# Kernel optimization log

Hardware: AMD Instinct MI355X
Metric: run time of the kernel (lower is better)

Reference implementation:

```python
import jax, jax.numpy as jnp
import numpy as np

C_IN = 128      # pair channel
C_HID = 32      # per-head hidden dim
H = 4           # heads
INF = 1e9
LN_EPS = 1e-5


def setup_inputs() -> dict:
    key = jax.random.key(0)
    ks = jax.random.split(key, 8)
    B, N = 1, 256
    s = 0.02
    return {
        "x": jax.random.normal(ks[0], (B, N, N, C_IN), dtype=jnp.float32),
        "mask": jnp.ones((B, N, N), dtype=jnp.float32),
        "ln_w": jnp.ones((C_IN,), dtype=jnp.float32),
        "ln_b": jnp.zeros((C_IN,), dtype=jnp.float32),
        "w_b": jax.random.normal(ks[1], (H, C_IN), dtype=jnp.float32) * s,      # triangle-bias linear (no bias)
        "w_q": jax.random.normal(ks[2], (H * C_HID, C_IN), dtype=jnp.float32) * s,
        "w_k": jax.random.normal(ks[3], (H * C_HID, C_IN), dtype=jnp.float32) * s,
        "w_v": jax.random.normal(ks[4], (H * C_HID, C_IN), dtype=jnp.float32) * s,
        "w_g": jax.random.normal(ks[5], (H * C_HID, C_IN), dtype=jnp.float32) * s,
        "b_g": jnp.ones((H * C_HID,), dtype=jnp.float32),
        "w_o": jax.random.normal(ks[6], (C_IN, H * C_HID), dtype=jnp.float32) * s,
        "b_o": jnp.zeros((C_IN,), dtype=jnp.float32),
    }


def reference(x, mask, ln_w, ln_b, w_b, w_q, w_k, w_v, w_g, b_g, w_o, b_o):
    # starting=True -> no transpose
    # LayerNorm over channel dim
    mu = jnp.mean(x, axis=-1, keepdims=True)
    var = jnp.var(x, axis=-1, keepdims=True)
    xn = (x - mu) * jax.lax.rsqrt(var + LN_EPS) * ln_w + ln_b            # [B,I,J,C]

    # mask bias: [B, I, 1, 1, J]
    mask_bias = (INF * (mask - 1.0))[..., :, None, None, :]

    # triangle bias: linear -> [B,I,J,H] -> permute -> [B,H,I,J] -> [B,1,H,I,J]
    tri_bias = jnp.einsum("bijc,hc->bhij", xn, w_b)[:, None]

    # QKV projections, per-head: weights reshaped to [H, D, C]
    Wq = w_q.reshape(H, C_HID, C_IN)
    Wk = w_k.reshape(H, C_HID, C_IN)
    Wv = w_v.reshape(H, C_HID, C_IN)
    scale = 1.0 / np.sqrt(C_HID)
    q = jnp.einsum("bijc,hdc->bihjd", xn, Wq) * scale                    # [B,I,H,J,D]
    k = jnp.einsum("bijc,hdc->bihjd", xn, Wk)
    v = jnp.einsum("bijc,hdc->bihjd", xn, Wv)

    # attention over the J (column) axis of each row i
    a = jnp.einsum("bihqd,bihkd->bihqk", q, k) + mask_bias + tri_bias    # [B,I,H,J,J]
    a = jax.nn.softmax(a, axis=-1)
    o = jnp.einsum("bihqk,bihkd->biqhd", a, v)                           # [B,I,J,H,D]

    # sigmoid gating
    g = jax.nn.sigmoid(jnp.einsum("bijc,ec->bije", xn, w_g) + b_g)       # [B,I,J,H*D]
    o = o.reshape(*o.shape[:-2], H * C_HID) * g

    # output projection
    return jnp.einsum("bije,ce->bijc", o, w_o) + b_o                     # [B,I,J,C_in]
```

## Files before the change

kernel.cpp:

```cpp
#include <hip/hip_runtime.h>

#define N 256
#define C 128
#define H 4
#define D 32
#define NP (N*N)
#define LN_EPS 1e-5f
#define LOG2E 1.4426950408889634f

using f32x4 = __attribute__((ext_vector_type(4))) float;
using bf8   = __attribute__((ext_vector_type(8))) short;
using u16x4 = __attribute__((ext_vector_type(4))) unsigned short;

__device__ __forceinline__ float bf2f(ushort u) {
    union { uint u; float f; } v; v.u = ((uint)u) << 16; return v.f;
}
__device__ __forceinline__ ushort f2bf(float f) {
    union { float f; uint u; } v; v.f = f;
    uint u = v.u;
    u += 0x7fffu + ((u >> 16) & 1u);
    return (ushort)(u >> 16);
}
__device__ __forceinline__ ushort f2bf_trunc(float f) {
    union { float f; uint u; } v; v.f = f;
    return (ushort)(v.u >> 16);
}

__global__ __launch_bounds__(256) void prep_weights(
    const float* __restrict__ wq, const float* __restrict__ wk,
    const float* __restrict__ wv, const float* __restrict__ wg,
    const float* __restrict__ wb, const float* __restrict__ wo,
    ushort* __restrict__ Wcat, ushort* __restrict__ WbPad, ushort* __restrict__ Wo)
{
    int t = blockIdx.x * 256 + threadIdx.x;
    const float scale = 0.17677669529663689f * LOG2E;
    float v;
    if (t < 16384)       v = wq[t] * scale;
    else if (t < 32768)  v = wk[t - 16384];
    else if (t < 49152)  v = wv[t - 32768];
    else                 v = wg[t - 49152];
    Wcat[t] = f2bf(v);
    if (t < 16384) Wo[t] = f2bf(wo[t]);
    if (t < 2048)  WbPad[t] = (t < 512) ? f2bf(wb[t]) : (ushort)0;
}

__global__ __launch_bounds__(512, 4) void ln_proj(
    const float* __restrict__ x, const float* __restrict__ lnw,
    const float* __restrict__ lnb, const ushort* __restrict__ Wcat,
    const ushort* __restrict__ WbPad, const float* __restrict__ bg,
    ushort* __restrict__ qb, ushort* __restrict__ kb,
    ushort* __restrict__ vbT, ushort* __restrict__ gate,
    ushort* __restrict__ tri_p)
{
    __shared__ ushort At[128 * 128];
    __shared__ ushort Bt[128 * 128];
    int mt = blockIdx.x;
    int t  = threadIdx.x;
    int wave = t >> 6, lane = t & 63;
    int lane32 = lane & 31, rsel = lane >> 5;

    {
        const float4 w4 = ((const float4*)lnw)[lane32];
        const float4 b4 = ((const float4*)lnb)[lane32];
        const float* xb = x + (size_t)mt * 128 * C;
        #pragma unroll
        for (int pp = 0; pp < 8; pp++) {
            int r = pp * 16 + wave * 2 + rsel;
            float4 xv = ((const float4*)(xb + r * C))[lane32];
            float s  = xv.x + xv.y + xv.z + xv.w;
            float ss = xv.x*xv.x + xv.y*xv.y + xv.z*xv.z + xv.w*xv.w;
            #pragma unroll
            for (int m = 1; m < 32; m <<= 1) {
                s  += __shfl_xor(s, m, 64);
                ss += __shfl_xor(ss, m, 64);
            }
            float mean = s * (1.f / 128.f);
            float var  = ss * (1.f / 128.f) - mean * mean;
            float rstd = rsqrtf(var + LN_EPS);
            u16x4 o;
            o[0] = f2bf((xv.x - mean) * rstd * w4.x + b4.x);
            o[1] = f2bf((xv.y - mean) * rstd * w4.y + b4.y);
            o[2] = f2bf((xv.z - mean) * rstd * w4.z + b4.z);
            o[3] = f2bf((xv.w - mean) * rstd * w4.w + b4.w);
            int c8 = lane32 >> 1;
            int chunk = r * 16 + (c8 ^ (r & 7));
            *(u16x4*)&At[chunk * 8 + (lane32 & 1) * 4] = o;
        }
    }
    __syncthreads();

    int lrow = lane & 15, quad = lane >> 4;
    int wr = wave >> 1, wc = wave & 1;

    bf8 afr[4][2];
    #pragma unroll
    for (int ks = 0; ks < 4; ks++) {
        int c8 = ks * 4 + quad;
        #pragma unroll
        for (int mi = 0; mi < 2; mi++) {
            int row = wr * 32 + mi * 16 + lrow;
            afr[ks][mi] = *(const bf8*)&At[(row * 16 + (c8 ^ (row & 7))) * 8];
        }
    }

    {
        f32x4 at0 = (f32x4){0.f,0.f,0.f,0.f}, at1 = (f32x4){0.f,0.f,0.f,0.f};
        #pragma unroll
        for (int ks = 0; ks < 4; ks++) {
            int c8 = ks * 4 + quad;
            bf8 bt = *(const bf8*)(WbPad + lrow * C + c8 * 8);
            at0 = __builtin_amdgcn_mfma_f32_16x16x32_bf16(afr[ks][0], bt, at0, 0, 0, 0);
            at1 = __builtin_amdgcn_mfma_f32_16x16x32_bf16(afr[ks][1], bt, at1, 0, 0, 0);
        }
        if (wc == 0 && lrow < 4) {
            int q = mt >> 1;
            int qc = q >> 4, quadq = (q >> 2) & 3, rr = q & 3;
            #pragma unroll
            for (int mi = 0; mi < 2; mi++) {
                #pragma unroll
                for (int r = 0; r < 4; r++) {
                    int k = (mt & 1) * 128 + wr * 32 + mi * 16 + quad * 4 + r;
                    int n = k >> 4, lk = k & 15;
                    int lanet = quadq * 16 + lk;
                    int v = n * 4 + rr, j = v >> 3, m2 = v & 7;
                    float val = (mi == 0) ? at0[r] : at1[r];
                    tri_p[lrow * 65536 + ((qc * 8 + j) * 64 + lanet) * 8 + m2] =
                        f2bf(val * LOG2E);
                }
            }
        }
    }

    uint4 breg[4];
    {
        const uint4* Bg = (const uint4*)Wcat;
        #pragma unroll
        for (int ii = 0; ii < 4; ii++) breg[ii] = Bg[t + ii * 512];
    }

    #pragma unroll 1
    for (int nt = 0; nt < 4; nt++) {
        __syncthreads();
        #pragma unroll
        for (int ii = 0; ii < 4; ii++) {
            int idx = t + ii * 512;
            int row = idx >> 4, c8 = idx & 15;
            ((uint4*)Bt)[row * 16 + (c8 ^ (row & 7))] = breg[ii];
        }
        __syncthreads();
        if (nt < 3) {
            const uint4* Bg = (const uint4*)(Wcat + (size_t)(nt + 1) * 128 * C);
            #pragma unroll
            for (int ii = 0; ii < 4; ii++) breg[ii] = Bg[t + ii * 512];
        }

        f32x4 acc[2][4];
        #pragma unroll
        for (int mi = 0; mi < 2; mi++)
            #pragma unroll
            for (int ni = 0; ni < 4; ni++) acc[mi][ni] = (f32x4){0.f, 0.f, 0.f, 0.f};

        #pragma unroll
        for (int ks = 0; ks < 4; ks++) {
            int c8 = ks * 4 + quad;
            bf8 b[4];
            #pragma unroll
            for (int ni = 0; ni < 4; ni++) {
                int row = wc * 64 + ni * 16 + lrow;
                b[ni] = *(const bf8*)&Bt[(row * 16 + (c8 ^ (row & 7))) * 8];
            }
            #pragma unroll
            for (int mi = 0; mi < 2; mi++)
                #pragma unroll
                for (int ni = 0; ni < 4; ni++)
                    acc[mi][ni] = __builtin_amdgcn_mfma_f32_16x16x32_bf16(afr[ks][mi], b[ni], acc[mi][ni], 0, 0, 0);
        }

        if (nt == 2) {
            __syncthreads();
            #pragma unroll
            for (int mi = 0; mi < 2; mi++) {
                #pragma unroll
                for (int ni = 0; ni < 4; ni++) {
                    int col = wc * 64 + ni * 16 + lrow;
                    #pragma unroll
                    for (int r = 0; r < 4; r++) {
                        int keyl = wr * 32 + mi * 16 + quad * 4 + r;
                        Bt[col * 128 + (keyl ^ (lrow << 3))] = f2bf(acc[mi][ni][r]);
                    }
                }
            }
            __syncthreads();
            int i_row = mt >> 1;
            #pragma unroll
            for (int itr = 0; itr < 4; itr++) {
                int oidx = itr * 512 + t;
                int col = oidx >> 4, kc = oidx & 15;
                bf8 val = *(const bf8*)&Bt[col * 128 + ((kc * 8) ^ ((col & 15) << 3))];
                *(bf8*)&vbT[(size_t)(i_row * 128 + col) * N + (mt & 1) * 128 + kc * 8] = val;
            }
        } else {
            ushort* dst = (nt == 0) ? qb : (nt == 1) ? kb : gate;
            bool gated = (nt == 3);
            #pragma unroll
            for (int mi = 0; mi < 2; mi++) {
                #pragma unroll
                for (int ni = 0; ni < 4; ni++) {
                    int col = wc * 64 + ni * 16 + lrow;
                    #pragma unroll
                    for (int r = 0; r < 4; r++) {
                        int row = mt * 128 + wr * 32 + mi * 16 + quad * 4 + r;
                        float vv = acc[mi][ni][r];
                        if (gated) vv = 1.f / (1.f + __expf(-(vv + bg[col])));
                        dst[(size_t)row * C + col] = f2bf(vv);
                    }
                }
            }
        }
    }
}

__global__ __launch_bounds__(512, 4) void attn_kernel(
    const ushort* __restrict__ qb, const ushort* __restrict__ kb,
    const ushort* __restrict__ vbT, const ushort* __restrict__ tri_p,
    const float* __restrict__ mask, ushort* __restrict__ ob)
{
    __shared__ ushort Kf[8192];
    __shared__ ushort Vf[8192];
    __shared__ ushort Pf[8][2048];

    int i  = blockIdx.x;
    int h  = blockIdx.y;
    int t  = threadIdx.x;
    int wave = t >> 6, lane = t & 63;
    int lrow = lane & 15, quad = lane >> 4;

    {
        const ushort* kt = kb + (size_t)(i * N) * C + h * D;
        #pragma unroll
        for (int it = 0; it < 2; it++) {
            int idx = it * 512 + t;
            int key = idx >> 2, d0 = (idx & 3) * 8;
            bf8 kv = *(const bf8*)(kt + (size_t)key * C + d0);
            int c = (idx >> 6) * 64 + (idx & 3) * 16 + ((idx >> 2) & 15);
            *(bf8*)&Kf[c * 8] = kv;
        }
    }
    {
        const ushort* vt = vbT + (size_t)((i * H + h) * D) * N;
        #pragma unroll
        for (int it = 0; it < 2; it++) {
            int idx = it * 512 + t;
            bf8 vv = *(const bf8*)(vt + idx * 8);
            int c = (idx >> 9) * 512 + ((idx >> 2) & 7) * 64 + (idx & 3) * 16 + ((idx >> 5) & 15);
            c ^= (c >> 6) & 7;
            *(bf8*)&Vf[c * 8] = vv;
        }
    }
    float mb[16];
    #pragma unroll
    for (int n = 0; n < 16; n++)
        mb[n] = (1e9f * LOG2E) * (mask[i * N + n * 16 + lrow] - 1.0f);
    __syncthreads();

    ushort* Pw = &Pf[wave][0];
    const ushort* trih = tri_p + (size_t)h * 65536;
    int pq = quad * 32 + (lrow & 7);
    int l3 = (lrow >> 3) & 1;

    #pragma unroll 1
    for (int cc = 0; cc < 2; cc++) {
        int qc = wave * 2 + cc;
        bf8 aq = *(const bf8*)(qb + (size_t)(i * N + qc * 16 + lrow) * C + h * D + quad * 8);
        float sum[4] = {0.f, 0.f, 0.f, 0.f};
        f32x4 o[2];
        o[0] = (f32x4){0.f, 0.f, 0.f, 0.f};
        o[1] = (f32x4){0.f, 0.f, 0.f, 0.f};

        #pragma unroll
        for (int half = 0; half < 2; half++) {
            f32x4 s8[8];
            #pragma unroll
            for (int n8 = 0; n8 < 8; n8++) {
                bf8 kf = *(const bf8*)&Kf[((half * 8 + n8) * 64 + lane) * 8];
                s8[n8] = __builtin_amdgcn_mfma_f32_16x16x32_bf16(
                    aq, kf, (f32x4){0.f, 0.f, 0.f, 0.f}, 0, 0, 0);
            }
            const ushort* tp = trih + ((size_t)(qc * 8 + half * 4) * 64 + lane) * 8;
            bf8 tf[4];
            #pragma unroll
            for (int jj = 0; jj < 4; jj++)
                tf[jj] = *(const bf8*)(tp + jj * 512);

            #pragma unroll
            for (int n8 = 0; n8 < 8; n8++) {
                int pa = (n8 >> 1) * 512 + (((n8 << 1) + l3) & 3) * 128 + pq;
                #pragma unroll
                for (int r = 0; r < 4; r++) {
                    float tb = bf2f(((const ushort*)&tf[n8 >> 1])[((n8 & 1) << 2) + r]);
                    float e  = exp2f(s8[n8][r] + tb + mb[half * 8 + n8]);
                    sum[r]  += e;
                    Pw[pa + r * 8] = f2bf_trunc(e);
                }
            }
            __asm__ volatile("s_waitcnt lgkmcnt(0)" ::: "memory");

            #pragma unroll
            for (int ks = 0; ks < 4; ks++) {
                bf8 ap = *(const bf8*)&Pw[(ks * 64 + lane) * 8];
                int ksg = half * 4 + ks;
                #pragma unroll
                for (int nv = 0; nv < 2; nv++) {
                    int c = nv * 512 + ksg * 64 + (lane ^ (ksg & 7));
                    bf8 bv = *(const bf8*)&Vf[c * 8];
                    o[nv] = __builtin_amdgcn_mfma_f32_16x16x32_bf16(ap, bv, o[nv], 0, 0, 0);
                }
            }
        }
        #pragma unroll
        for (int r = 0; r < 4; r++) {
            float s = sum[r];
            s += __shfl_xor(s, 1, 64);
            s += __shfl_xor(s, 2, 64);
            s += __shfl_xor(s, 4, 64);
            s += __shfl_xor(s, 8, 64);
            sum[r] = 1.f / s;
        }
        #pragma unroll
        for (int nv = 0; nv < 2; nv++) {
            int d = nv * 16 + lrow;
            #pragma unroll
            for (int r = 0; r < 4; r++) {
                int qg = qc * 16 + quad * 4 + r;
                ob[(size_t)(i * N + qg) * C + h * D + d] = f2bf(o[nv][r] * sum[r]);
            }
        }
    }
}

__global__ __launch_bounds__(512, 4) void out_gemm(
    const ushort* __restrict__ ob, const ushort* __restrict__ gate,
    const ushort* __restrict__ Wo, const float* __restrict__ bo,
    float* __restrict__ out)
{
    __shared__ ushort At[128 * 128];
    __shared__ ushort Bt[128 * 128];
    int mt = blockIdx.x;
    int t  = threadIdx.x;

    const uint4* Og = (const uint4*)(ob   + (size_t)mt * 128 * C);
    const uint4* Gg = (const uint4*)(gate + (size_t)mt * 128 * C);
    const uint4* Bg = (const uint4*)Wo;
    #pragma unroll
    for (int ii = 0; ii < 4; ii++) {
        int idx = t + ii * 512;
        int row = idx >> 4, c8 = idx & 15;
        int sc = row * 16 + (c8 ^ (row & 7));
        uint4 o4 = Og[idx], g4 = Gg[idx], r4;
        const ushort* os = (const ushort*)&o4;
        const ushort* gs = (const ushort*)&g4;
        ushort* rs = (ushort*)&r4;
        #pragma unroll
        for (int j = 0; j < 8; j++) rs[j] = f2bf(bf2f(os[j]) * bf2f(gs[j]));
        ((uint4*)At)[sc] = r4;
        ((uint4*)Bt)[sc] = Bg[idx];
    }
    __syncthreads();

    int wave = t >> 6, lane = t & 63;
    int lrow = lane & 15, quad = lane >> 4;
    int wr = wave >> 1, wc = wave & 1;

    f32x4 acc[2][4];
    #pragma unroll
    for (int mi = 0; mi < 2; mi++)
        #pragma unroll
        for (int ni = 0; ni < 4; ni++) acc[mi][ni] = (f32x4){0.f, 0.f, 0.f, 0.f};

    #pragma unroll
    for (int ks = 0; ks < 4; ks++) {
        int c8 = ks * 4 + quad;
        bf8 a[2], b[4];
        #pragma unroll
        for (int mi = 0; mi < 2; mi++) {
            int row = wr * 32 + mi * 16 + lrow;
            a[mi] = *(const bf8*)&At[(row * 16 + (c8 ^ (row & 7))) * 8];
        }
        #pragma unroll
        for (int ni = 0; ni < 4; ni++) {
            int row = wc * 64 + ni * 16 + lrow;
            b[ni] = *(const bf8*)&Bt[(row * 16 + (c8 ^ (row & 7))) * 8];
        }
        #pragma unroll
        for (int mi = 0; mi < 2; mi++)
            #pragma unroll
            for (int ni = 0; ni < 4; ni++)
                acc[mi][ni] = __builtin_amdgcn_mfma_f32_16x16x32_bf16(a[mi], b[ni], acc[mi][ni], 0, 0, 0);
    }

    #pragma unroll
    for (int mi = 0; mi < 2; mi++) {
        #pragma unroll
        for (int ni = 0; ni < 4; ni++) {
            int col = wc * 64 + ni * 16 + lrow;
            float bias = bo[col];
            #pragma unroll
            for (int r = 0; r < 4; r++) {
                int row = mt * 128 + wr * 32 + mi * 16 + quad * 4 + r;
                out[(size_t)row * C + col] = acc[mi][ni][r] + bias;
            }
        }
    }
}

extern "C" void kernel_launch(void* const* d_in, const int* in_sizes, int n_in,
                              void* d_out, int out_size, void* d_ws, size_t ws_size,
                              hipStream_t stream)
{
    const float* x    = (const float*)d_in[0];
    const float* mask = (const float*)d_in[1];
    const float* lnw  = (const float*)d_in[2];
    const float* lnb  = (const float*)d_in[3];
    const float* wb   = (const float*)d_in[4];
    const float* wq   = (const float*)d_in[5];
    const float* wk   = (const float*)d_in[6];
    const float* wv   = (const float*)d_in[7];
    const float* wg   = (const float*)d_in[8];
    const float* bg   = (const float*)d_in[9];
    const float* wo   = (const float*)d_in[10];
    const float* bo   = (const float*)d_in[11];
    float* out = (float*)d_out;

    uintptr_t w = (uintptr_t)d_ws;
    ushort* qb    = (ushort*)w; w += (size_t)NP * C * 2;
    ushort* kb    = (ushort*)w; w += (size_t)NP * C * 2;
    ushort* vbT   = (ushort*)w; w += (size_t)NP * C * 2;
    ushort* gate  = (ushort*)w; w += (size_t)NP * C * 2;
    ushort* ob    = (ushort*)w; w += (size_t)NP * C * 2;
    ushort* tri_p = (ushort*)w; w += (size_t)H * NP * 2;
    ushort* Wcat  = (ushort*)w; w += 512 * 128 * 2;
    ushort* WbPad = (ushort*)w; w += 16 * 128 * 2;
    ushort* Wo    = (ushort*)w; w += 128 * 128 * 2;

    prep_weights<<<256, 256, 0, stream>>>(wq, wk, wv, wg, wb, wo, Wcat, WbPad, Wo);
    ln_proj<<<NP / 128, 512, 0, stream>>>(x, lnw, lnb, Wcat, WbPad, bg,
                                          qb, kb, vbT, gate, tri_p);
    attn_kernel<<<dim3(N, H), 512, 0, stream>>>(qb, kb, vbT, tri_p, mask, ob);
    out_gemm<<<NP / 128, 512, 0, stream>>>(ob, gate, Wo, bo, out);
}
```

Measured before the change: 199.5 us.

## Shrink ln_proj tile to 64 rows, read weights from global, stage coalesced stores

The LayerNorm+projection kernel now processes 64 rows per block instead of 128, doubling the grid and cutting LDS use to a single 16 KB buffer. Weight tiles are read directly from global/L2 instead of being staged through shared memory. Output tiles for q/k/gate go through LDS so each lane writes a 16-byte vector store instead of scattered 2-byte stores, and x loads are batched before the reductions. It trades more global weight reads and extra barriers for higher occupancy and better store coalescing.

```diff
diff --git a/kernel.cpp b/kernel.cpp
--- a/kernel.cpp
+++ b/kernel.cpp
@@ -52,8 +52,7 @@
     ushort* __restrict__ vbT, ushort* __restrict__ gate,
     ushort* __restrict__ tri_p)
 {
-    __shared__ ushort At[128 * 128];
-    __shared__ ushort Bt[128 * 128];
+    __shared__ ushort At[64 * 128];
     int mt = blockIdx.x;
     int t  = threadIdx.x;
     int wave = t >> 6, lane = t & 63;
@@ -62,13 +61,19 @@
     {
         const float4 w4 = ((const float4*)lnw)[lane32];
         const float4 b4 = ((const float4*)lnb)[lane32];
-        const float* xb = x + (size_t)mt * 128 * C;
-        #pragma unroll
-        for (int pp = 0; pp < 8; pp++) {
+        const float* xb = x + (size_t)mt * 64 * C;
+        float4 xv[4];
+        #pragma unroll
+        for (int pp = 0; pp < 4; pp++) {
             int r = pp * 16 + wave * 2 + rsel;
-            float4 xv = ((const float4*)(xb + r * C))[lane32];
-            float s  = xv.x + xv.y + xv.z + xv.w;
-            float ss = xv.x*xv.x + xv.y*xv.y + xv.z*xv.z + xv.w*xv.w;
+            xv[pp] = ((const float4*)(xb + r * C))[lane32];
+        }
+        #pragma unroll
+        for (int pp = 0; pp < 4; pp++) {
+            int r = pp * 16 + wave * 2 + rsel;
+            float4 v = xv[pp];
+            float s  = v.x + v.y + v.z + v.w;
+            float ss = v.x*v.x + v.y*v.y + v.z*v.z + v.w*v.w;
             #pragma unroll
             for (int m = 1; m < 32; m <<= 1) {
                 s  += __shfl_xor(s, m, 64);
@@ -78,10 +83,10 @@
             float var  = ss * (1.f / 128.f) - mean * mean;
             float rstd = rsqrtf(var + LN_EPS);
             u16x4 o;
-            o[0] = f2bf((xv.x - mean) * rstd * w4.x + b4.x);
-            o[1] = f2bf((xv.y - mean) * rstd * w4.y + b4.y);
-            o[2] = f2bf((xv.z - mean) * rstd * w4.z + b4.z);
-            o[3] = f2bf((xv.w - mean) * rstd * w4.w + b4.w);
+            o[0] = f2bf((v.x - mean) * rstd * w4.x + b4.x);
+            o[1] = f2bf((v.y - mean) * rstd * w4.y + b4.y);
+            o[2] = f2bf((v.z - mean) * rstd * w4.z + b4.z);
+            o[3] = f2bf((v.w - mean) * rstd * w4.w + b4.w);
             int c8 = lane32 >> 1;
             int chunk = r * 16 + (c8 ^ (r & 7));
             *(u16x4*)&At[chunk * 8 + (lane32 & 1) * 4] = o;
@@ -90,7 +95,7 @@
     __syncthreads();
 
     int lrow = lane & 15, quad = lane >> 4;
-    int wr = wave >> 1, wc = wave & 1;
+    int wr = wave >> 2, wc = wave & 3;
 
     bf8 afr[4][2];
     #pragma unroll
@@ -103,26 +108,25 @@
         }
     }
 
-    {
+    if (wc == 0) {
         f32x4 at0 = (f32x4){0.f,0.f,0.f,0.f}, at1 = (f32x4){0.f,0.f,0.f,0.f};
         #pragma unroll
         for (int ks = 0; ks < 4; ks++) {
-            int c8 = ks * 4 + quad;
-            bf8 bt = *(const bf8*)(WbPad + lrow * C + c8 * 8);
+            bf8 bt = *(const bf8*)(WbPad + lrow * C + (ks * 4 + quad) * 8);
             at0 = __builtin_amdgcn_mfma_f32_16x16x32_bf16(afr[ks][0], bt, at0, 0, 0, 0);
             at1 = __builtin_amdgcn_mfma_f32_16x16x32_bf16(afr[ks][1], bt, at1, 0, 0, 0);
         }
-        if (wc == 0 && lrow < 4) {
-            int q = mt >> 1;
+        if (lrow < 4) {
+            int q = mt >> 2;
             int qc = q >> 4, quadq = (q >> 2) & 3, rr = q & 3;
             #pragma unroll
             for (int mi = 0; mi < 2; mi++) {
                 #pragma unroll
                 for (int r = 0; r < 4; r++) {
-                    int k = (mt & 1) * 128 + wr * 32 + mi * 16 + quad * 4 + r;
+                    int k = (mt & 3) * 64 + wr * 32 + mi * 16 + quad * 4 + r;
                     int n = k >> 4, lk = k & 15;
                     int lanet = quadq * 16 + lk;
-                    int v = n * 4 + rr, j = v >> 3, m2 = v & 7;
+                    int v2 = n * 4 + rr, j = v2 >> 3, m2 = v2 & 7;
                     float val = (mi == 0) ? at0[r] : at1[r];
                     tri_p[lrow * 65536 + ((qc * 8 + j) * 64 + lanet) * 8 + m2] =
                         f2bf(val * LOG2E);
@@ -131,90 +135,75 @@
         }
     }
 
-    uint4 breg[4];
-    {
-        const uint4* Bg = (const uint4*)Wcat;
-        #pragma unroll
-        for (int ii = 0; ii < 4; ii++) breg[ii] = Bg[t + ii * 512];
-    }
-
     #pragma unroll 1
     for (int nt = 0; nt < 4; nt++) {
-        __syncthreads();
-        #pragma unroll
-        for (int ii = 0; ii < 4; ii++) {
-            int idx = t + ii * 512;
-            int row = idx >> 4, c8 = idx & 15;
-            ((uint4*)Bt)[row * 16 + (c8 ^ (row & 7))] = breg[ii];
-        }
-        __syncthreads();
-        if (nt < 3) {
-            const uint4* Bg = (const uint4*)(Wcat + (size_t)(nt + 1) * 128 * C);
-            #pragma unroll
-            for (int ii = 0; ii < 4; ii++) breg[ii] = Bg[t + ii * 512];
-        }
-
-        f32x4 acc[2][4];
+        const ushort* Wt = Wcat + (size_t)nt * 128 * C;
+        f32x4 acc[2][2];
         #pragma unroll
         for (int mi = 0; mi < 2; mi++)
             #pragma unroll
-            for (int ni = 0; ni < 4; ni++) acc[mi][ni] = (f32x4){0.f, 0.f, 0.f, 0.f};
+            for (int ni = 0; ni < 2; ni++) acc[mi][ni] = (f32x4){0.f, 0.f, 0.f, 0.f};
 
         #pragma unroll
         for (int ks = 0; ks < 4; ks++) {
             int c8 = ks * 4 + quad;
-            bf8 b[4];
-            #pragma unroll
-            for (int ni = 0; ni < 4; ni++) {
-                int row = wc * 64 + ni * 16 + lrow;
-                b[ni] = *(const bf8*)&Bt[(row * 16 + (c8 ^ (row & 7))) * 8];
-            }
-            #pragma unroll
-            for (int mi = 0; mi < 2; mi++)
-                #pragma unroll
-                for (int ni = 0; ni < 4; ni++)
-                    acc[mi][ni] = __builtin_amdgcn_mfma_f32_16x16x32_bf16(afr[ks][mi], b[ni], acc[mi][ni], 0, 0, 0);
-        }
-
+            bf8 b0 = *(const bf8*)(Wt + (size_t)(wc * 32 + lrow)      * C + c8 * 8);
+            bf8 b1 = *(const bf8*)(Wt + (size_t)(wc * 32 + 16 + lrow) * C + c8 * 8);
+            acc[0][0] = __builtin_amdgcn_mfma_f32_16x16x32_bf16(afr[ks][0], b0, acc[0][0], 0, 0, 0);
+            acc[0][1] = __builtin_amdgcn_mfma_f32_16x16x32_bf16(afr[ks][0], b1, acc[0][1], 0, 0, 0);
+            acc[1][0] = __builtin_amdgcn_mfma_f32_16x16x32_bf16(afr[ks][1], b0, acc[1][0], 0, 0, 0);
+            acc[1][1] = __builtin_amdgcn_mfma_f32_16x16x32_bf16(afr[ks][1], b1, acc[1][1], 0, 0, 0);
+        }
+
+        __syncthreads();
         if (nt == 2) {
-            __syncthreads();
             #pragma unroll
             for (int mi = 0; mi < 2; mi++) {
                 #pragma unroll
-                for (int ni = 0; ni < 4; ni++) {
-                    int col = wc * 64 + ni * 16 + lrow;
+                for (int ni = 0; ni < 2; ni++) {
+                    int col = wc * 32 + ni * 16 + lrow;
                     #pragma unroll
                     for (int r = 0; r < 4; r++) {
                         int keyl = wr * 32 + mi * 16 + quad * 4 + r;
-                        Bt[col * 128 + (keyl ^ (lrow << 3))] = f2bf(acc[mi][ni][r]);
+                        At[col * 64 + (keyl ^ ((col & 7) << 3))] = f2bf(acc[mi][ni][r]);
                     }
                 }
             }
             __syncthreads();
-            int i_row = mt >> 1;
-            #pragma unroll
-            for (int itr = 0; itr < 4; itr++) {
+            int i_row = mt >> 2, kq = mt & 3;
+            #pragma unroll
+            for (int itr = 0; itr < 2; itr++) {
                 int oidx = itr * 512 + t;
-                int col = oidx >> 4, kc = oidx & 15;
-                bf8 val = *(const bf8*)&Bt[col * 128 + ((kc * 8) ^ ((col & 15) << 3))];
-                *(bf8*)&vbT[(size_t)(i_row * 128 + col) * N + (mt & 1) * 128 + kc * 8] = val;
+                int col = oidx >> 3, kc = oidx & 7;
+                bf8 val = *(const bf8*)&At[col * 64 + ((kc * 8) ^ ((col & 7) << 3))];
+                *(bf8*)&vbT[(size_t)(i_row * 128 + col) * N + kq * 64 + kc * 8] = val;
             }
         } else {
             ushort* dst = (nt == 0) ? qb : (nt == 1) ? kb : gate;
-            bool gated = (nt == 3);
+            float g0 = 0.f, g1 = 0.f;
+            if (nt == 3) { g0 = bg[wc * 32 + lrow]; g1 = bg[wc * 32 + 16 + lrow]; }
             #pragma unroll
             for (int mi = 0; mi < 2; mi++) {
                 #pragma unroll
-                for (int ni = 0; ni < 4; ni++) {
-                    int col = wc * 64 + ni * 16 + lrow;
+                for (int ni = 0; ni < 2; ni++) {
+                    int col = wc * 32 + ni * 16 + lrow;
                     #pragma unroll
                     for (int r = 0; r < 4; r++) {
-                        int row = mt * 128 + wr * 32 + mi * 16 + quad * 4 + r;
+                        int row = wr * 32 + mi * 16 + quad * 4 + r;
                         float vv = acc[mi][ni][r];
-                        if (gated) vv = 1.f / (1.f + __expf(-(vv + bg[col])));
-                        dst[(size_t)row * C + col] = f2bf(vv);
+                        if (nt == 3)
+                            vv = 1.f / (1.f + __expf(-(vv + ((ni == 0) ? g0 : g1))));
+                        At[(row * 16 + ((col >> 3) ^ (row & 7))) * 8 + (col & 7)] = f2bf(vv);
                     }
                 }
+            }
+            __syncthreads();
+            #pragma unroll
+            for (int itr = 0; itr < 2; itr++) {
+                int oidx = itr * 512 + t;
+                int row = oidx >> 4, c8 = oidx & 15;
+                bf8 val = *(const bf8*)&At[(row * 16 + (c8 ^ (row & 7))) * 8];
+                *(bf8*)&dst[(size_t)(mt * 64 + row) * C + c8 * 8] = val;
             }
         }
     }
@@ -443,8 +432,8 @@
     ushort* Wo    = (ushort*)w; w += 128 * 128 * 2;
 
     prep_weights<<<256, 256, 0, stream>>>(wq, wk, wv, wg, wb, wo, Wcat, WbPad, Wo);
-    ln_proj<<<NP / 128, 512, 0, stream>>>(x, lnw, lnb, Wcat, WbPad, bg,
-                                          qb, kb, vbT, gate, tri_p);
+    ln_proj<<<NP / 64, 512, 0, stream>>>(x, lnw, lnb, Wcat, WbPad, bg,
+                                         qb, kb, vbT, gate, tri_p);
     attn_kernel<<<dim3(N, H), 512, 0, stream>>>(qb, kb, vbT, tri_p, mask, ob);
     out_gemm<<<NP / 128, 512, 0, stream>>>(ob, gate, Wo, bo, out);
 }
```

Result: faster. 184.6 us (-7.5%).
